# Kernel tuning notes

Hardware: AMD Instinct MI355X
Metric: run time of the kernel (lower is better)

The kernel has to match this reference:

```python
import jax, jax.numpy as jnp
import numpy as np

D_MODEL = 768
N_HEADS = 12
D_K = D_MODEL // N_HEADS
NEG_INF = -1e9


def setup_inputs() -> dict:
    key = jax.random.key(0)
    ks = jax.random.split(key, 7)
    B, S = 4, 2048
    x = jax.random.normal(ks[0], (B, S, D_MODEL), dtype=jnp.float32)
    # causal mask, broadcastable to [B, H, S, S]
    mask = jnp.tril(jnp.ones((S, S), dtype=bool))[None, None, :, :]
    scale = 1.0 / np.sqrt(D_MODEL)
    Wq = jax.random.normal(ks[1], (D_MODEL, D_MODEL), dtype=jnp.float32) * scale
    bq = jnp.zeros((D_MODEL,), dtype=jnp.float32)
    Wk = jax.random.normal(ks[2], (D_MODEL, D_MODEL), dtype=jnp.float32) * scale
    bk = jnp.zeros((D_MODEL,), dtype=jnp.float32)
    Wv = jax.random.normal(ks[3], (D_MODEL, D_MODEL), dtype=jnp.float32) * scale
    bv = jnp.zeros((D_MODEL,), dtype=jnp.float32)
    return {"x": x, "mask": mask, "Wq": Wq, "bq": bq, "Wk": Wk, "bk": bk, "Wv": Wv, "bv": bv}


def reference(x, mask, Wq, bq, Wk, bk, Wv, bv):
    B, S, _ = x.shape
    # projections (torch Linear: y = x @ W.T + b)
    q = (x @ Wq.T + bq).reshape(B, S, N_HEADS, D_K)
    k = (x @ Wk.T + bk).reshape(B, S, N_HEADS, D_K)
    v = (x @ Wv.T + bv).reshape(B, S, N_HEADS, D_K)
    # scores: [B, H, S, S]
    scores = jnp.einsum("bqhd,bkhd->bhqk", q, k) / jnp.sqrt(jnp.float32(D_K))
    scores = jnp.where(mask, scores, NEG_INF)
    probs = jax.nn.softmax(scores, axis=-1)
    # attention: [B, H, S, D_K] -> [B, S, d_model]
    attn = jnp.einsum("bhqk,bkhd->bqhd", probs, v).reshape(B, S, D_MODEL)
    return attn
```

## Files before the change

### kernel.cpp

```cpp
#include <hip/hip_runtime.h>


#define S_LEN 2048
#define BATCH 4
#define HEADS 12
#define DM 768
#define DK 64
#define BH (BATCH*HEADS)
#define MROWS (BATCH*S_LEN)

typedef __attribute__((ext_vector_type(8))) short short8;
typedef __attribute__((ext_vector_type(4))) float floatx4;
typedef __attribute__((address_space(3))) unsigned char lds_byte;
typedef __attribute__((address_space(1))) const unsigned char glob_byte;

__device__ __forceinline__ unsigned short f2bf(float f) {
  union { float f; unsigned int u; } a; a.f = f;
  unsigned int u = a.u;
  return (unsigned short)((u + 0x7fffu + ((u >> 16) & 1u)) >> 16);
}

__global__ void cast_f32_bf16(const float* __restrict__ src,
                              unsigned short* __restrict__ dst, int n) {
  int i = (blockIdx.x * blockDim.x + threadIdx.x) * 4;
  if (i < n) {
    float4 v = *(const float4*)(src + i);
    ushort4 o;
    o.x = f2bf(v.x); o.y = f2bf(v.y); o.z = f2bf(v.z); o.w = f2bf(v.w);
    *(ushort4*)(dst + i) = o;
  }
}

__global__ void cast_w3(const float* __restrict__ w0, const float* __restrict__ w1,
                        const float* __restrict__ w2, unsigned short* __restrict__ dst,
                        int n) {
  const float* src = (blockIdx.y == 0) ? w0 : (blockIdx.y == 1) ? w1 : w2;
  int i = (blockIdx.x * blockDim.x + threadIdx.x) * 4;
  if (i < n) {
    float4 v = *(const float4*)(src + i);
    ushort4 o;
    o.x = f2bf(v.x); o.y = f2bf(v.y); o.z = f2bf(v.z); o.w = f2bf(v.w);
    *(ushort4*)(dst + (size_t)blockIdx.y * n + i) = o;
  }
}

__global__ __launch_bounds__(256) void qkv_gemm(
    const unsigned short* __restrict__ xb,
    const unsigned short* __restrict__ wb,
    const float* __restrict__ bq, const float* __restrict__ bk,
    const float* __restrict__ bv,
    unsigned short* __restrict__ qo,
    unsigned short* __restrict__ ko,
    unsigned short* __restrict__ vto) {
  __shared__ unsigned short a_lds[128 * 32];
  __shared__ unsigned short b_lds[128 * 32];
  const int mat = blockIdx.z;
  const int tid = threadIdx.x;
  const int wave = tid >> 6, lane = tid & 63, quad = lane >> 4, ln = lane & 15;
  const int wm = wave & 1, wn = wave >> 1;
  const int m_blk = blockIdx.x * 128, n_blk = blockIdx.y * 128;
  const unsigned short* w = wb + (size_t)mat * DM * DM;

  const int srow = lane >> 2, schunk = lane & 3;

  const floatx4 fz = {0.f, 0.f, 0.f, 0.f};
  floatx4 acc[4][4];
#pragma unroll
  for (int mg = 0; mg < 4; mg++)
#pragma unroll
    for (int c = 0; c < 4; c++) acc[mg][c] = fz;

  for (int k0 = 0; k0 < DM; k0 += 32) {
#pragma unroll
    for (int j = 0; j < 2; j++) {
      int row = wave * 32 + j * 16 + srow;
      __builtin_amdgcn_global_load_lds(
          (glob_byte*)(xb + (size_t)(m_blk + row) * DM + k0 + schunk * 8),
          (lds_byte*)(a_lds + (size_t)(wave * 32 + j * 16) * 32), 16, 0, 0);
      __builtin_amdgcn_global_load_lds(
          (glob_byte*)(w + (size_t)(n_blk + row) * DM + k0 + schunk * 8),
          (lds_byte*)(b_lds + (size_t)(wave * 32 + j * 16) * 32), 16, 0, 0);
    }
    __syncthreads();

    short8 af[4], bf[4];
#pragma unroll
    for (int mg = 0; mg < 4; mg++)
      af[mg] = *(const short8*)(a_lds + (wm * 64 + mg * 16 + ln) * 32 + quad * 8);
#pragma unroll
    for (int c = 0; c < 4; c++)
      bf[c] = *(const short8*)(b_lds + (wn * 64 + c * 16 + ln) * 32 + quad * 8);
#pragma unroll
    for (int mg = 0; mg < 4; mg++)
#pragma unroll
      for (int c = 0; c < 4; c++)
        acc[mg][c] = __builtin_amdgcn_mfma_f32_16x16x32_bf16(af[mg], bf[c], acc[mg][c], 0, 0, 0);
    __syncthreads();
  }

  const float* bias = (mat == 0) ? bq : (mat == 1) ? bk : bv;
  const int m_base = m_blk + wm * 64, n_base = n_blk + wn * 64;
#pragma unroll
  for (int mg = 0; mg < 4; mg++)
#pragma unroll
    for (int c = 0; c < 4; c++) {
      int gn = n_base + c * 16 + ln;
      int hd = gn >> 6, d = gn & 63;
      float bias_v = bias[gn];
      int gm0 = m_base + mg * 16 + quad * 4;
      int bb = gm0 >> 11, s0 = gm0 & (S_LEN - 1);
      if (mat == 2) {
        ushort4 pk;
        pk.x = f2bf(acc[mg][c][0] + bias_v);
        pk.y = f2bf(acc[mg][c][1] + bias_v);
        pk.z = f2bf(acc[mg][c][2] + bias_v);
        pk.w = f2bf(acc[mg][c][3] + bias_v);
        *(ushort4*)(vto + (((size_t)(bb * HEADS + hd)) * DK + d) * S_LEN + s0) = pk;
      } else {
        unsigned short* dst = (mat == 0 ? qo : ko) +
            (((size_t)(bb * HEADS + hd)) * S_LEN + s0) * DK + d;
#pragma unroll
        for (int r = 0; r < 4; r++)
          dst[(size_t)r * DK] = f2bf(acc[mg][c][r] + bias_v);
      }
    }
}

__global__ __launch_bounds__(128) void flash_attn(
    const unsigned short* __restrict__ q,
    const unsigned short* __restrict__ k,
    const unsigned short* __restrict__ vt,
    float* __restrict__ out) {
  __shared__ unsigned short p_lds[2][32 * 64];
  const int id = blockIdx.x;
  const int bh = id % BH;
  const int qt = (S_LEN / 64 - 1) - (id / BH);
  const int q0 = qt * 64;
  const int tid = threadIdx.x;
  const int wave = tid >> 6, lane = tid & 63, quad = lane >> 4, ln = lane & 15;
  unsigned short* pl = p_lds[wave];
  const unsigned short* qp = q  + (size_t)bh * S_LEN * DK;
  const unsigned short* kp = k  + (size_t)bh * S_LEN * DK;
  const unsigned short* vp = vt + (size_t)bh * DK * S_LEN;
  const int qr_base = q0 + wave * 32;

  short8 aq[2][2];
#pragma unroll
  for (int h = 0; h < 2; h++)
#pragma unroll
    for (int s = 0; s < 2; s++)
      aq[h][s] = *(const short8*)(qp + (size_t)(qr_base + h * 16 + ln) * DK + s * 32 + quad * 8);

  const floatx4 fz = {0.f, 0.f, 0.f, 0.f};
  floatx4 o[2][4];
  float l_part[2][4];
#pragma unroll
  for (int h = 0; h < 2; h++)
#pragma unroll
    for (int r = 0; r < 4; r++) {
      o[h][0] = fz; o[h][1] = fz; o[h][2] = fz; o[h][3] = fz;
      l_part[h][r] = 0.f;
    }

  const int kend = qr_base + 32;
  for (int k0 = 0; k0 < kend; k0 += 64) {
    short8 kf[4][2];
#pragma unroll
    for (int kg = 0; kg < 4; kg++)
#pragma unroll
      for (int s = 0; s < 2; s++)
        kf[kg][s] = *(const short8*)(kp + (size_t)(k0 + kg * 16 + ln) * DK + s * 32 + quad * 8);

    floatx4 sc[2][4];
#pragma unroll
    for (int h = 0; h < 2; h++)
#pragma unroll
      for (int kg = 0; kg < 4; kg++) {
        floatx4 t = __builtin_amdgcn_mfma_f32_16x16x32_bf16(aq[h][0], kf[kg][0], fz, 0, 0, 0);
        sc[h][kg] = __builtin_amdgcn_mfma_f32_16x16x32_bf16(aq[h][1], kf[kg][1], t, 0, 0, 0);
      }

    const bool domask = (k0 + 63 > qr_base);
#pragma unroll
    for (int h = 0; h < 2; h++) {
#pragma unroll
      for (int kg = 0; kg < 4; kg++) {
        int key = k0 + kg * 16 + ln;
#pragma unroll
        for (int r = 0; r < 4; r++) {
          float p = __expf(sc[h][kg][r] * 0.125f);
          if (domask) {
            int qr = qr_base + h * 16 + quad * 4 + r;
            p = (key <= qr) ? p : 0.f;
          }
          l_part[h][r] += p;
          int row = h * 16 + quad * 4 + r;
          int col = kg * 16 + ln;
          pl[row * 64 + (((col >> 3) ^ (row & 7)) * 8) + (col & 7)] = f2bf(p);
        }
      }
    }

    short8 ap[2][2];
#pragma unroll
    for (int h = 0; h < 2; h++)
#pragma unroll
      for (int s = 0; s < 2; s++)
        ap[h][s] = *(const short8*)(pl + (h * 16 + ln) * 64 + (((s * 4 + quad) ^ (ln & 7)) * 8));

    short8 vf[4][2];
#pragma unroll
    for (int dg = 0; dg < 4; dg++)
#pragma unroll
      for (int s = 0; s < 2; s++)
        vf[dg][s] = *(const short8*)(vp + (size_t)(dg * 16 + ln) * S_LEN + k0 + s * 32 + quad * 8);
#pragma unroll
    for (int h = 0; h < 2; h++)
#pragma unroll
      for (int dg = 0; dg < 4; dg++) {
        o[h][dg] = __builtin_amdgcn_mfma_f32_16x16x32_bf16(ap[h][0], vf[dg][0], o[h][dg], 0, 0, 0);
        o[h][dg] = __builtin_amdgcn_mfma_f32_16x16x32_bf16(ap[h][1], vf[dg][1], o[h][dg], 0, 0, 0);
      }
  }

  const int b = bh / HEADS, hd = bh % HEADS;
#pragma unroll
  for (int h = 0; h < 2; h++)
#pragma unroll
    for (int r = 0; r < 4; r++) {
      float l = l_part[h][r];
      l += __shfl_xor(l, 1);
      l += __shfl_xor(l, 2);
      l += __shfl_xor(l, 4);
      l += __shfl_xor(l, 8);
      float inv = 1.f / l;
      int qr = qr_base + h * 16 + quad * 4 + r;
      float* orow = out + ((size_t)(b * S_LEN + qr)) * DM + hd * DK;
      orow[ln]      = o[h][0][r] * inv;
      orow[16 + ln] = o[h][1][r] * inv;
      orow[32 + ln] = o[h][2][r] * inv;
      orow[48 + ln] = o[h][3][r] * inv;
    }
}

extern "C" void kernel_launch(void* const* d_in, const int* in_sizes, int n_in,
                              void* d_out, int out_size, void* d_ws, size_t ws_size,
                              hipStream_t stream) {
  const float* x  = (const float*)d_in[0];
  const float* Wq = (const float*)d_in[2];
  const float* bq = (const float*)d_in[3];
  const float* Wk = (const float*)d_in[4];
  const float* bk = (const float*)d_in[5];
  const float* Wv = (const float*)d_in[6];
  const float* bv = (const float*)d_in[7];
  float* out = (float*)d_out;

  const int NX = MROWS * DM;
  const int NW = DM * DM;
  unsigned short* xb = (unsigned short*)d_ws;
  unsigned short* wb = xb + NX;
  unsigned short* qo = wb + 3 * NW;
  unsigned short* ko = qo + (size_t)BH * S_LEN * DK;
  unsigned short* vt = ko + (size_t)BH * S_LEN * DK;

  cast_f32_bf16<<<(NX / 4 + 255) / 256, 256, 0, stream>>>(x, xb, NX);
  cast_w3<<<dim3((NW / 4 + 255) / 256, 3), 256, 0, stream>>>(Wq, Wk, Wv, wb, NW);

  qkv_gemm<<<dim3(MROWS / 128, DM / 128, 3), 256, 0, stream>>>(
      xb, wb, bq, bk, bv, qo, ko, vt);

  flash_attn<<<dim3((S_LEN / 64) * BH), 128, 0, stream>>>(qo, ko, vt, out);
}
```

Baseline: 254.8 us.

## Fold softmax scale into Q, unroll attention loop with double-buffered P tiles

Pre-multiplies Q by log2(e)/sqrt(dk) in the projection epilogue so attention can use exp2f directly, removing a multiply per score. The attention key loop is refactored into an inlined step function, unrolled by two with separate per-wave P buffers in LDS, and the V loads are hoisted next to the K loads so both can be in flight together. Launch bounds now request 3 blocks per CU. The added register pressure from earlier V loads and the unroll may limit occupancy or cause spills. Q rounding to bf16 now happens after scaling, which changes numerics slightly.

```diff
diff --git a/kernel.cpp b/kernel.cpp
--- a/kernel.cpp
+++ b/kernel.cpp
@@ -1,4 +1,5 @@
 #include <hip/hip_runtime.h>
+#include <math.h>
 
 
 #define S_LEN 2048
@@ -8,6 +9,7 @@
 #define DK 64
 #define BH (BATCH*HEADS)
 #define MROWS (BATCH*S_LEN)
+#define QSCALE 0.1803368801111244f
 
 typedef __attribute__((ext_vector_type(8))) short short8;
 typedef __attribute__((ext_vector_type(4))) float floatx4;
@@ -60,7 +62,6 @@
   const int wm = wave & 1, wn = wave >> 1;
   const int m_blk = blockIdx.x * 128, n_blk = blockIdx.y * 128;
   const unsigned short* w = wb + (size_t)mat * DM * DM;
-
   const int srow = lane >> 2, schunk = lane & 3;
 
   const floatx4 fz = {0.f, 0.f, 0.f, 0.f};
@@ -99,6 +100,7 @@
   }
 
   const float* bias = (mat == 0) ? bq : (mat == 1) ? bk : bv;
+  const float oscale = (mat == 0) ? QSCALE : 1.0f;
   const int m_base = m_blk + wm * 64, n_base = n_blk + wn * 64;
 #pragma unroll
   for (int mg = 0; mg < 4; mg++)
@@ -106,7 +108,7 @@
     for (int c = 0; c < 4; c++) {
       int gn = n_base + c * 16 + ln;
       int hd = gn >> 6, d = gn & 63;
-      float bias_v = bias[gn];
+      float bias_v = bias[gn] * oscale;
       int gm0 = m_base + mg * 16 + quad * 4;
       int bb = gm0 >> 11, s0 = gm0 & (S_LEN - 1);
       if (mat == 2) {
@@ -121,24 +123,86 @@
             (((size_t)(bb * HEADS + hd)) * S_LEN + s0) * DK + d;
 #pragma unroll
         for (int r = 0; r < 4; r++)
-          dst[(size_t)r * DK] = f2bf(acc[mg][c][r] + bias_v);
+          dst[(size_t)r * DK] = f2bf(acc[mg][c][r] * oscale + bias_v);
       }
     }
 }
 
-__global__ __launch_bounds__(128) void flash_attn(
+__device__ __forceinline__ void attn_step(
+    int k0, int qr_base, int quad, int ln,
+    const unsigned short* __restrict__ kp, const unsigned short* __restrict__ vp,
+    unsigned short* __restrict__ pl,
+    const short8 (&aq)[2][2], floatx4 (&o)[2][4], float (&l_part)[2][4]) {
+  const floatx4 fz = {0.f, 0.f, 0.f, 0.f};
+  short8 kf[4][2], vf[4][2];
+#pragma unroll
+  for (int kg = 0; kg < 4; kg++)
+#pragma unroll
+    for (int s = 0; s < 2; s++) {
+      kf[kg][s] = *(const short8*)(kp + (size_t)(k0 + kg * 16 + ln) * DK + s * 32 + quad * 8);
+      vf[kg][s] = *(const short8*)(vp + (size_t)(kg * 16 + ln) * S_LEN + k0 + s * 32 + quad * 8);
+    }
+
+  floatx4 sc[2][4];
+#pragma unroll
+  for (int h = 0; h < 2; h++)
+#pragma unroll
+    for (int kg = 0; kg < 4; kg++) {
+      floatx4 t = __builtin_amdgcn_mfma_f32_16x16x32_bf16(aq[h][0], kf[kg][0], fz, 0, 0, 0);
+      sc[h][kg] = __builtin_amdgcn_mfma_f32_16x16x32_bf16(aq[h][1], kf[kg][1], t, 0, 0, 0);
+    }
+
+  const bool domask = (k0 + 63 > qr_base);
+#pragma unroll
+  for (int h = 0; h < 2; h++) {
+#pragma unroll
+    for (int kg = 0; kg < 4; kg++) {
+      int key = k0 + kg * 16 + ln;
+#pragma unroll
+      for (int r = 0; r < 4; r++) {
+        float p = exp2f(sc[h][kg][r]);
+        if (domask) {
+          int qr = qr_base + h * 16 + quad * 4 + r;
+          p = (key <= qr) ? p : 0.f;
+        }
+        l_part[h][r] += p;
+        int row = h * 16 + quad * 4 + r;
+        int col = kg * 16 + ln;
+        pl[row * 64 + (((col >> 3) ^ (row & 7)) * 8) + (col & 7)] = f2bf(p);
+      }
+    }
+  }
+
+  short8 ap[2][2];
+#pragma unroll
+  for (int h = 0; h < 2; h++)
+#pragma unroll
+    for (int s = 0; s < 2; s++)
+      ap[h][s] = *(const short8*)(pl + (h * 16 + ln) * 64 + (((s * 4 + quad) ^ (ln & 7)) * 8));
+
+#pragma unroll
+  for (int h = 0; h < 2; h++)
+#pragma unroll
+    for (int dg = 0; dg < 4; dg++) {
+      o[h][dg] = __builtin_amdgcn_mfma_f32_16x16x32_bf16(ap[h][0], vf[dg][0], o[h][dg], 0, 0, 0);
+      o[h][dg] = __builtin_amdgcn_mfma_f32_16x16x32_bf16(ap[h][1], vf[dg][1], o[h][dg], 0, 0, 0);
+    }
+}
+
+__global__ __launch_bounds__(128, 3) void flash_attn(
     const unsigned short* __restrict__ q,
     const unsigned short* __restrict__ k,
     const unsigned short* __restrict__ vt,
     float* __restrict__ out) {
-  __shared__ unsigned short p_lds[2][32 * 64];
+  __shared__ unsigned short p_lds[2][2][32 * 64];
   const int id = blockIdx.x;
   const int bh = id % BH;
   const int qt = (S_LEN / 64 - 1) - (id / BH);
   const int q0 = qt * 64;
   const int tid = threadIdx.x;
   const int wave = tid >> 6, lane = tid & 63, quad = lane >> 4, ln = lane & 15;
-  unsigned short* pl = p_lds[wave];
+  unsigned short* pl0 = p_lds[wave][0];
+  unsigned short* pl1 = p_lds[wave][1];
   const unsigned short* qp = q  + (size_t)bh * S_LEN * DK;
   const unsigned short* kp = k  + (size_t)bh * S_LEN * DK;
   const unsigned short* vp = vt + (size_t)bh * DK * S_LEN;
@@ -163,65 +227,14 @@
     }
 
   const int kend = qr_base + 32;
-  for (int k0 = 0; k0 < kend; k0 += 64) {
-    short8 kf[4][2];
-#pragma unroll
-    for (int kg = 0; kg < 4; kg++)
-#pragma unroll
-      for (int s = 0; s < 2; s++)
-        kf[kg][s] = *(const short8*)(kp + (size_t)(k0 + kg * 16 + ln) * DK + s * 32 + quad * 8);
-
-    floatx4 sc[2][4];
-#pragma unroll
-    for (int h = 0; h < 2; h++)
-#pragma unroll
-      for (int kg = 0; kg < 4; kg++) {
-        floatx4 t = __builtin_amdgcn_mfma_f32_16x16x32_bf16(aq[h][0], kf[kg][0], fz, 0, 0, 0);
-        sc[h][kg] = __builtin_amdgcn_mfma_f32_16x16x32_bf16(aq[h][1], kf[kg][1], t, 0, 0, 0);
-      }
-
-    const bool domask = (k0 + 63 > qr_base);
-#pragma unroll
-    for (int h = 0; h < 2; h++) {
-#pragma unroll
-      for (int kg = 0; kg < 4; kg++) {
-        int key = k0 + kg * 16 + ln;
-#pragma unroll
-        for (int r = 0; r < 4; r++) {
-          float p = __expf(sc[h][kg][r] * 0.125f);
-          if (domask) {
-            int qr = qr_base + h * 16 + quad * 4 + r;
-            p = (key <= qr) ? p : 0.f;
-          }
-          l_part[h][r] += p;
-          int row = h * 16 + quad * 4 + r;
-          int col = kg * 16 + ln;
-          pl[row * 64 + (((col >> 3) ^ (row & 7)) * 8) + (col & 7)] = f2bf(p);
-        }
-      }
-    }
-
-    short8 ap[2][2];
-#pragma unroll
-    for (int h = 0; h < 2; h++)
-#pragma unroll
-      for (int s = 0; s < 2; s++)
-        ap[h][s] = *(const short8*)(pl + (h * 16 + ln) * 64 + (((s * 4 + quad) ^ (ln & 7)) * 8));
-
-    short8 vf[4][2];
-#pragma unroll
-    for (int dg = 0; dg < 4; dg++)
-#pragma unroll
-      for (int s = 0; s < 2; s++)
-        vf[dg][s] = *(const short8*)(vp + (size_t)(dg * 16 + ln) * S_LEN + k0 + s * 32 + quad * 8);
-#pragma unroll
-    for (int h = 0; h < 2; h++)
-#pragma unroll
-      for (int dg = 0; dg < 4; dg++) {
-        o[h][dg] = __builtin_amdgcn_mfma_f32_16x16x32_bf16(ap[h][0], vf[dg][0], o[h][dg], 0, 0, 0);
-        o[h][dg] = __builtin_amdgcn_mfma_f32_16x16x32_bf16(ap[h][1], vf[dg][1], o[h][dg], 0, 0, 0);
-      }
-  }
+  int k0 = 0;
+  while (k0 + 128 <= kend) {
+    attn_step(k0,      qr_base, quad, ln, kp, vp, pl0, aq, o, l_part);
+    attn_step(k0 + 64, qr_base, quad, ln, kp, vp, pl1, aq, o, l_part);
+    k0 += 128;
+  }
+  for (int t = 0; k0 < kend; k0 += 64, t ^= 1)
+    attn_step(k0, qr_base, quad, ln, kp, vp, t ? pl1 : pl0, aq, o, l_part);
 
   const int b = bh / HEADS, hd = bh % HEADS;
 #pragma unroll
```

New measurement: 392.5 us. +54.0%, slower.

## Schedule attention tiles per wave via atomic queue and fold softmax scale into Q

Applied to the files above, without the earlier changes.

The attention kernel now hands out 32-row causal query tiles to individual waves. Each wave takes its next tile from a global atomic counter, longest tiles first, instead of each block owning a fixed 64-row tile, which is meant to even out the causal work imbalance and the tail. The 1/sqrt(dk)*log2(e) factor is folded into the Q projection epilogue, so the softmax uses exp2f with no per-element multiply. This adds one memset launch and one atomic per tile. The larger scale on Q may slightly change bf16 rounding of Q.

```diff
diff --git a/kernel.cpp b/kernel.cpp
--- a/kernel.cpp
+++ b/kernel.cpp
@@ -1,4 +1,5 @@
 #include <hip/hip_runtime.h>
+#include <math.h>
 
 
 #define S_LEN 2048
@@ -8,6 +9,8 @@
 #define DK 64
 #define BH (BATCH*HEADS)
 #define MROWS (BATCH*S_LEN)
+#define QSCALE 0.1803368801111244f
+#define N_ITEMS ((S_LEN/32)*BH)
 
 typedef __attribute__((ext_vector_type(8))) short short8;
 typedef __attribute__((ext_vector_type(4))) float floatx4;
@@ -60,7 +63,6 @@
   const int wm = wave & 1, wn = wave >> 1;
   const int m_blk = blockIdx.x * 128, n_blk = blockIdx.y * 128;
   const unsigned short* w = wb + (size_t)mat * DM * DM;
-
   const int srow = lane >> 2, schunk = lane & 3;
 
   const floatx4 fz = {0.f, 0.f, 0.f, 0.f};
@@ -99,6 +101,7 @@
   }
 
   const float* bias = (mat == 0) ? bq : (mat == 1) ? bk : bv;
+  const float oscale = (mat == 0) ? QSCALE : 1.0f;
   const int m_base = m_blk + wm * 64, n_base = n_blk + wn * 64;
 #pragma unroll
   for (int mg = 0; mg < 4; mg++)
@@ -106,7 +109,7 @@
     for (int c = 0; c < 4; c++) {
       int gn = n_base + c * 16 + ln;
       int hd = gn >> 6, d = gn & 63;
-      float bias_v = bias[gn];
+      float bias_v = bias[gn] * oscale;
       int gm0 = m_base + mg * 16 + quad * 4;
       int bb = gm0 >> 11, s0 = gm0 & (S_LEN - 1);
       if (mat == 2) {
@@ -121,7 +124,7 @@
             (((size_t)(bb * HEADS + hd)) * S_LEN + s0) * DK + d;
 #pragma unroll
         for (int r = 0; r < 4; r++)
-          dst[(size_t)r * DK] = f2bf(acc[mg][c][r] + bias_v);
+          dst[(size_t)r * DK] = f2bf(acc[mg][c][r] * oscale + bias_v);
       }
     }
 }
@@ -130,117 +133,124 @@
     const unsigned short* __restrict__ q,
     const unsigned short* __restrict__ k,
     const unsigned short* __restrict__ vt,
-    float* __restrict__ out) {
+    float* __restrict__ out,
+    unsigned int* __restrict__ work_ctr) {
   __shared__ unsigned short p_lds[2][32 * 64];
-  const int id = blockIdx.x;
-  const int bh = id % BH;
-  const int qt = (S_LEN / 64 - 1) - (id / BH);
-  const int q0 = qt * 64;
   const int tid = threadIdx.x;
   const int wave = tid >> 6, lane = tid & 63, quad = lane >> 4, ln = lane & 15;
   unsigned short* pl = p_lds[wave];
-  const unsigned short* qp = q  + (size_t)bh * S_LEN * DK;
-  const unsigned short* kp = k  + (size_t)bh * S_LEN * DK;
-  const unsigned short* vp = vt + (size_t)bh * DK * S_LEN;
-  const int qr_base = q0 + wave * 32;
-
-  short8 aq[2][2];
-#pragma unroll
-  for (int h = 0; h < 2; h++)
-#pragma unroll
-    for (int s = 0; s < 2; s++)
-      aq[h][s] = *(const short8*)(qp + (size_t)(qr_base + h * 16 + ln) * DK + s * 32 + quad * 8);
-
   const floatx4 fz = {0.f, 0.f, 0.f, 0.f};
-  floatx4 o[2][4];
-  float l_part[2][4];
-#pragma unroll
-  for (int h = 0; h < 2; h++)
-#pragma unroll
-    for (int r = 0; r < 4; r++) {
-      o[h][0] = fz; o[h][1] = fz; o[h][2] = fz; o[h][3] = fz;
-      l_part[h][r] = 0.f;
+
+  for (;;) {
+    unsigned int item = 0;
+    if (lane == 0) item = atomicAdd(work_ctr, 1u);
+    item = __shfl((int)item, 0);
+    if (item >= N_ITEMS) return;
+
+    const int bh = item % BH;
+    const int t  = (S_LEN / 32 - 1) - (int)(item / BH);
+    const int qr_base = t * 32;
+    const unsigned short* qp = q  + (size_t)bh * S_LEN * DK;
+    const unsigned short* kp = k  + (size_t)bh * S_LEN * DK;
+    const unsigned short* vp = vt + (size_t)bh * DK * S_LEN;
+
+    short8 aq[2][2];
+#pragma unroll
+    for (int h = 0; h < 2; h++)
+#pragma unroll
+      for (int s = 0; s < 2; s++)
+        aq[h][s] = *(const short8*)(qp + (size_t)(qr_base + h * 16 + ln) * DK + s * 32 + quad * 8);
+
+    floatx4 o[2][4];
+    float l_part[2][4];
+#pragma unroll
+    for (int h = 0; h < 2; h++)
+#pragma unroll
+      for (int r = 0; r < 4; r++) {
+        o[h][0] = fz; o[h][1] = fz; o[h][2] = fz; o[h][3] = fz;
+        l_part[h][r] = 0.f;
+      }
+
+    const int kend = qr_base + 32;
+    for (int k0 = 0; k0 < kend; k0 += 64) {
+      short8 kf[4][2];
+#pragma unroll
+      for (int kg = 0; kg < 4; kg++)
+#pragma unroll
+        for (int s = 0; s < 2; s++)
+          kf[kg][s] = *(const short8*)(kp + (size_t)(k0 + kg * 16 + ln) * DK + s * 32 + quad * 8);
+
+      floatx4 sc[2][4];
+#pragma unroll
+      for (int h = 0; h < 2; h++)
+#pragma unroll
+        for (int kg = 0; kg < 4; kg++) {
+          floatx4 tt = __builtin_amdgcn_mfma_f32_16x16x32_bf16(aq[h][0], kf[kg][0], fz, 0, 0, 0);
+          sc[h][kg] = __builtin_amdgcn_mfma_f32_16x16x32_bf16(aq[h][1], kf[kg][1], tt, 0, 0, 0);
+        }
+
+      const bool domask = (k0 + 63 > qr_base);
+#pragma unroll
+      for (int h = 0; h < 2; h++) {
+#pragma unroll
+        for (int kg = 0; kg < 4; kg++) {
+          int key = k0 + kg * 16 + ln;
+#pragma unroll
+          for (int r = 0; r < 4; r++) {
+            float p = exp2f(sc[h][kg][r]);
+            if (domask) {
+              int qr = qr_base + h * 16 + quad * 4 + r;
+              p = (key <= qr) ? p : 0.f;
+            }
+            l_part[h][r] += p;
+            int row = h * 16 + quad * 4 + r;
+            int col = kg * 16 + ln;
+            pl[row * 64 + (((col >> 3) ^ (row & 7)) * 8) + (col & 7)] = f2bf(p);
+          }
+        }
+      }
+
+      short8 ap[2][2];
+#pragma unroll
+      for (int h = 0; h < 2; h++)
+#pragma unroll
+        for (int s = 0; s < 2; s++)
+          ap[h][s] = *(const short8*)(pl + (h * 16 + ln) * 64 + (((s * 4 + quad) ^ (ln & 7)) * 8));
+
+      short8 vf[4][2];
+#pragma unroll
+      for (int dg = 0; dg < 4; dg++)
+#pragma unroll
+        for (int s = 0; s < 2; s++)
+          vf[dg][s] = *(const short8*)(vp + (size_t)(dg * 16 + ln) * S_LEN + k0 + s * 32 + quad * 8);
+#pragma unroll
+      for (int h = 0; h < 2; h++)
+#pragma unroll
+        for (int dg = 0; dg < 4; dg++) {
+          o[h][dg] = __builtin_amdgcn_mfma_f32_16x16x32_bf16(ap[h][0], vf[dg][0], o[h][dg], 0, 0, 0);
+          o[h][dg] = __builtin_amdgcn_mfma_f32_16x16x32_bf16(ap[h][1], vf[dg][1], o[h][dg], 0, 0, 0);
+        }
     }
 
-  const int kend = qr_base + 32;
-  for (int k0 = 0; k0 < kend; k0 += 64) {
-    short8 kf[4][2];
-#pragma unroll
-    for (int kg = 0; kg < 4; kg++)
-#pragma unroll
-      for (int s = 0; s < 2; s++)
-        kf[kg][s] = *(const short8*)(kp + (size_t)(k0 + kg * 16 + ln) * DK + s * 32 + quad * 8);
-
-    floatx4 sc[2][4];
+    const int b = bh / HEADS, hd = bh % HEADS;
 #pragma unroll
     for (int h = 0; h < 2; h++)
 #pragma unroll
-      for (int kg = 0; kg < 4; kg++) {
-        floatx4 t = __builtin_amdgcn_mfma_f32_16x16x32_bf16(aq[h][0], kf[kg][0], fz, 0, 0, 0);
-        sc[h][kg] = __builtin_amdgcn_mfma_f32_16x16x32_bf16(aq[h][1], kf[kg][1], t, 0, 0, 0);
-      }
-
-    const bool domask = (k0 + 63 > qr_base);
-#pragma unroll
-    for (int h = 0; h < 2; h++) {
-#pragma unroll
-      for (int kg = 0; kg < 4; kg++) {
-        int key = k0 + kg * 16 + ln;
-#pragma unroll
-        for (int r = 0; r < 4; r++) {
-          float p = __expf(sc[h][kg][r] * 0.125f);
-          if (domask) {
-            int qr = qr_base + h * 16 + quad * 4 + r;
-            p = (key <= qr) ? p : 0.f;
-          }
-          l_part[h][r] += p;
-          int row = h * 16 + quad * 4 + r;
-          int col = kg * 16 + ln;
-          pl[row * 64 + (((col >> 3) ^ (row & 7)) * 8) + (col & 7)] = f2bf(p);
-        }
-      }
-    }
-
-    short8 ap[2][2];
-#pragma unroll
-    for (int h = 0; h < 2; h++)
-#pragma unroll
-      for (int s = 0; s < 2; s++)
-        ap[h][s] = *(const short8*)(pl + (h * 16 + ln) * 64 + (((s * 4 + quad) ^ (ln & 7)) * 8));
-
-    short8 vf[4][2];
-#pragma unroll
-    for (int dg = 0; dg < 4; dg++)
-#pragma unroll
-      for (int s = 0; s < 2; s++)
-        vf[dg][s] = *(const short8*)(vp + (size_t)(dg * 16 + ln) * S_LEN + k0 + s * 32 + quad * 8);
-#pragma unroll
-    for (int h = 0; h < 2; h++)
-#pragma unroll
-      for (int dg = 0; dg < 4; dg++) {
-        o[h][dg] = __builtin_amdgcn_mfma_f32_16x16x32_bf16(ap[h][0], vf[dg][0], o[h][dg], 0, 0, 0);
-        o[h][dg] = __builtin_amdgcn_mfma_f32_16x16x32_bf16(ap[h][1], vf[dg][1], o[h][dg], 0, 0, 0);
-      }
-  }
-
-  const int b = bh / HEADS, hd = bh % HEADS;
-#pragma unroll
-  for (int h = 0; h < 2; h++)
-#pragma unroll
-    for (int r = 0; r < 4; r++) {
-      float l = l_part[h][r];
-      l += __shfl_xor(l, 1);
-      l += __shfl_xor(l, 2);
-      l += __shfl_xor(l, 4);
-      l += __shfl_xor(l, 8);
-      float inv = 1.f / l;
-      int qr = qr_base + h * 16 + quad * 4 + r;
-      float* orow = out + ((size_t)(b * S_LEN + qr)) * DM + hd * DK;
-      orow[ln]      = o[h][0][r] * inv;
-      orow[16 + ln] = o[h][1][r] * inv;
-      orow[32 + ln] = o[h][2][r] * inv;
-      orow[48 + ln] = o[h][3][r] * inv;
-    }
+      for (int r = 0; r < 4; r++) {
+        float l = l_part[h][r];
+        l += __shfl_xor(l, 1);
+        l += __shfl_xor(l, 2);
+        l += __shfl_xor(l, 4);
+        l += __shfl_xor(l, 8);
+        float inv = 1.f / l;
+        int qr = qr_base + h * 16 + quad * 4 + r;
+        float* orow = out + ((size_t)(b * S_LEN + qr)) * DM + hd * DK;
+        orow[ln]      = o[h][0][r] * inv;
+        orow[16 + ln] = o[h][1][r] * inv;
+        orow[32 + ln] = o[h][2][r] * inv;
+        orow[48 + ln] = o[h][3][r] * inv;
+      }
+  }
 }
 
 extern "C" void kernel_launch(void* const* d_in, const int* in_sizes, int n_in,
@@ -262,6 +272,9 @@
   unsigned short* qo = wb + 3 * NW;
   unsigned short* ko = qo + (size_t)BH * S_LEN * DK;
   unsigned short* vt = ko + (size_t)BH * S_LEN * DK;
+  unsigned int* ctr = (unsigned int*)(vt + (size_t)BH * S_LEN * DK);
+
+  hipMemsetAsync(ctr, 0, sizeof(unsigned int), stream);
 
   cast_f32_bf16<<<(NX / 4 + 255) / 256, 256, 0, stream>>>(x, xb, NX);
   cast_w3<<<dim3((NW / 4 + 255) / 256, 3), 256, 0, stream>>>(Wq, Wk, Wv, wb, NW);
@@ -269,5 +282,5 @@
   qkv_gemm<<<dim3(MROWS / 128, DM / 128, 3), 256, 0, stream>>>(
       xb, wb, bq, bk, bv, qo, ko, vt);
 
-  flash_attn<<<dim3((S_LEN / 64) * BH), 128, 0, stream>>>(qo, ko, vt, out);
-}
+  flash_attn<<<dim3(N_ITEMS / 2), 128, 0, stream>>>(qo, ko, vt, out, ctr);
+}
```

New measurement: 305.8 us. 20.0% more time.

## Rebalance causal attention with paired 16-row tiles per wave and fold scale into Q

Applied to the files above, without the earlier changes.

Each wave now processes two 16-row query tiles, one short and one long (ti and 127-ti), so every wave does the same causal work. Heads are mapped across 768 blocks of 4 waves, grouped so that block-adjacent work shares a head. The softmax scale and log2(e) are folded into the Q projection so the inner loop uses exp2f directly. Probabilities are converted to bf16 by truncation rather than rounding. Using 16-row tiles halves K/V reuse per wave compared with 32-row tiles, which raises global load traffic.

```diff
diff --git a/kernel.cpp b/kernel.cpp
--- a/kernel.cpp
+++ b/kernel.cpp
@@ -1,4 +1,5 @@
 #include <hip/hip_runtime.h>
+#include <math.h>
 
 
 #define S_LEN 2048
@@ -8,6 +9,7 @@
 #define DK 64
 #define BH (BATCH*HEADS)
 #define MROWS (BATCH*S_LEN)
+#define QSCALE 0.1803368801111244f
 
 typedef __attribute__((ext_vector_type(8))) short short8;
 typedef __attribute__((ext_vector_type(4))) float floatx4;
@@ -18,6 +20,10 @@
   union { float f; unsigned int u; } a; a.f = f;
   unsigned int u = a.u;
   return (unsigned short)((u + 0x7fffu + ((u >> 16) & 1u)) >> 16);
+}
+__device__ __forceinline__ unsigned short f2bf_rtz(float f) {
+  union { float f; unsigned int u; } a; a.f = f;
+  return (unsigned short)(a.u >> 16);
 }
 
 __global__ void cast_f32_bf16(const float* __restrict__ src,
@@ -60,7 +66,6 @@
   const int wm = wave & 1, wn = wave >> 1;
   const int m_blk = blockIdx.x * 128, n_blk = blockIdx.y * 128;
   const unsigned short* w = wb + (size_t)mat * DM * DM;
-
   const int srow = lane >> 2, schunk = lane & 3;
 
   const floatx4 fz = {0.f, 0.f, 0.f, 0.f};
@@ -99,6 +104,7 @@
   }
 
   const float* bias = (mat == 0) ? bq : (mat == 1) ? bk : bv;
+  const float oscale = (mat == 0) ? QSCALE : 1.0f;
   const int m_base = m_blk + wm * 64, n_base = n_blk + wn * 64;
 #pragma unroll
   for (int mg = 0; mg < 4; mg++)
@@ -106,7 +112,7 @@
     for (int c = 0; c < 4; c++) {
       int gn = n_base + c * 16 + ln;
       int hd = gn >> 6, d = gn & 63;
-      float bias_v = bias[gn];
+      float bias_v = bias[gn] * oscale;
       int gm0 = m_base + mg * 16 + quad * 4;
       int bb = gm0 >> 11, s0 = gm0 & (S_LEN - 1);
       if (mat == 2) {
@@ -121,126 +127,112 @@
             (((size_t)(bb * HEADS + hd)) * S_LEN + s0) * DK + d;
 #pragma unroll
         for (int r = 0; r < 4; r++)
-          dst[(size_t)r * DK] = f2bf(acc[mg][c][r] + bias_v);
-      }
-    }
-}
-
-__global__ __launch_bounds__(128) void flash_attn(
+          dst[(size_t)r * DK] = f2bf(acc[mg][c][r] * oscale + bias_v);
+      }
+    }
+}
+
+__global__ __launch_bounds__(256) void flash_attn(
     const unsigned short* __restrict__ q,
     const unsigned short* __restrict__ k,
     const unsigned short* __restrict__ vt,
     float* __restrict__ out) {
-  __shared__ unsigned short p_lds[2][32 * 64];
-  const int id = blockIdx.x;
-  const int bh = id % BH;
-  const int qt = (S_LEN / 64 - 1) - (id / BH);
-  const int q0 = qt * 64;
+  __shared__ unsigned short p_lds[4][16 * 64];
   const int tid = threadIdx.x;
   const int wave = tid >> 6, lane = tid & 63, quad = lane >> 4, ln = lane & 15;
   unsigned short* pl = p_lds[wave];
+  const int g = blockIdx.x & 7;
+  const int s = blockIdx.x >> 3;
+  const int p = s * 4 + wave;
+  const int bh = g + 8 * (p % 6);
+  const int ti = p / 6;
   const unsigned short* qp = q  + (size_t)bh * S_LEN * DK;
   const unsigned short* kp = k  + (size_t)bh * S_LEN * DK;
   const unsigned short* vp = vt + (size_t)bh * DK * S_LEN;
-  const int qr_base = q0 + wave * 32;
-
-  short8 aq[2][2];
-#pragma unroll
-  for (int h = 0; h < 2; h++)
-#pragma unroll
-    for (int s = 0; s < 2; s++)
-      aq[h][s] = *(const short8*)(qp + (size_t)(qr_base + h * 16 + ln) * DK + s * 32 + quad * 8);
-
   const floatx4 fz = {0.f, 0.f, 0.f, 0.f};
-  floatx4 o[2][4];
-  float l_part[2][4];
-#pragma unroll
-  for (int h = 0; h < 2; h++)
-#pragma unroll
-    for (int r = 0; r < 4; r++) {
-      o[h][0] = fz; o[h][1] = fz; o[h][2] = fz; o[h][3] = fz;
-      l_part[h][r] = 0.f;
-    }
-
-  const int kend = qr_base + 32;
-  for (int k0 = 0; k0 < kend; k0 += 64) {
-    short8 kf[4][2];
-#pragma unroll
-    for (int kg = 0; kg < 4; kg++)
-#pragma unroll
-      for (int s = 0; s < 2; s++)
-        kf[kg][s] = *(const short8*)(kp + (size_t)(k0 + kg * 16 + ln) * DK + s * 32 + quad * 8);
-
-    floatx4 sc[2][4];
-#pragma unroll
-    for (int h = 0; h < 2; h++)
+  const int b = bh / HEADS, hd = bh % HEADS;
+
+#pragma unroll
+  for (int job = 0; job < 2; job++) {
+    const int t16 = job ? (127 - ti) : ti;
+    const int qr_base = t16 * 16;
+
+    short8 aq[2];
+#pragma unroll
+    for (int ss = 0; ss < 2; ss++)
+      aq[ss] = *(const short8*)(qp + (size_t)(qr_base + ln) * DK + ss * 32 + quad * 8);
+
+    floatx4 o[4] = {fz, fz, fz, fz};
+    float l_part[4] = {0.f, 0.f, 0.f, 0.f};
+
+    const int kend = qr_base + 16;
+    for (int k0 = 0; k0 < kend; k0 += 64) {
+      short8 kf[4][2];
+#pragma unroll
+      for (int kg = 0; kg < 4; kg++)
+#pragma unroll
+        for (int ss = 0; ss < 2; ss++)
+          kf[kg][ss] = *(const short8*)(kp + (size_t)(k0 + kg * 16 + ln) * DK + ss * 32 + quad * 8);
+
+      floatx4 sc[4];
 #pragma unroll
       for (int kg = 0; kg < 4; kg++) {
-        floatx4 t = __builtin_amdgcn_mfma_f32_16x16x32_bf16(aq[h][0], kf[kg][0], fz, 0, 0, 0);
-        sc[h][kg] = __builtin_amdgcn_mfma_f32_16x16x32_bf16(aq[h][1], kf[kg][1], t, 0, 0, 0);
-      }
-
-    const bool domask = (k0 + 63 > qr_base);
-#pragma unroll
-    for (int h = 0; h < 2; h++) {
+        floatx4 tt = __builtin_amdgcn_mfma_f32_16x16x32_bf16(aq[0], kf[kg][0], fz, 0, 0, 0);
+        sc[kg] = __builtin_amdgcn_mfma_f32_16x16x32_bf16(aq[1], kf[kg][1], tt, 0, 0, 0);
+      }
+
+      const bool domask = (k0 + 63 > qr_base);
 #pragma unroll
       for (int kg = 0; kg < 4; kg++) {
         int key = k0 + kg * 16 + ln;
 #pragma unroll
         for (int r = 0; r < 4; r++) {
-          float p = __expf(sc[h][kg][r] * 0.125f);
+          float pv = exp2f(sc[kg][r]);
           if (domask) {
-            int qr = qr_base + h * 16 + quad * 4 + r;
-            p = (key <= qr) ? p : 0.f;
+            int qr = qr_base + quad * 4 + r;
+            pv = (key <= qr) ? pv : 0.f;
           }
-          l_part[h][r] += p;
-          int row = h * 16 + quad * 4 + r;
+          l_part[r] += pv;
+          int row = quad * 4 + r;
           int col = kg * 16 + ln;
-          pl[row * 64 + (((col >> 3) ^ (row & 7)) * 8) + (col & 7)] = f2bf(p);
+          pl[row * 64 + (((col >> 3) ^ row) & 7) * 8 + (col & 7)] = f2bf_rtz(pv);
         }
       }
-    }
-
-    short8 ap[2][2];
-#pragma unroll
-    for (int h = 0; h < 2; h++)
-#pragma unroll
-      for (int s = 0; s < 2; s++)
-        ap[h][s] = *(const short8*)(pl + (h * 16 + ln) * 64 + (((s * 4 + quad) ^ (ln & 7)) * 8));
-
-    short8 vf[4][2];
-#pragma unroll
-    for (int dg = 0; dg < 4; dg++)
-#pragma unroll
-      for (int s = 0; s < 2; s++)
-        vf[dg][s] = *(const short8*)(vp + (size_t)(dg * 16 + ln) * S_LEN + k0 + s * 32 + quad * 8);
-#pragma unroll
-    for (int h = 0; h < 2; h++)
+
+      short8 ap[2];
+#pragma unroll
+      for (int ss = 0; ss < 2; ss++)
+        ap[ss] = *(const short8*)(pl + ln * 64 + (((ss * 4 + quad) ^ ln) & 7) * 8);
+
+      short8 vf[4][2];
+#pragma unroll
+      for (int dg = 0; dg < 4; dg++)
+#pragma unroll
+        for (int ss = 0; ss < 2; ss++)
+          vf[dg][ss] = *(const short8*)(vp + (size_t)(dg * 16 + ln) * S_LEN + k0 + ss * 32 + quad * 8);
 #pragma unroll
       for (int dg = 0; dg < 4; dg++) {
-        o[h][dg] = __builtin_amdgcn_mfma_f32_16x16x32_bf16(ap[h][0], vf[dg][0], o[h][dg], 0, 0, 0);
-        o[h][dg] = __builtin_amdgcn_mfma_f32_16x16x32_bf16(ap[h][1], vf[dg][1], o[h][dg], 0, 0, 0);
-      }
-  }
-
-  const int b = bh / HEADS, hd = bh % HEADS;
-#pragma unroll
-  for (int h = 0; h < 2; h++)
+        o[dg] = __builtin_amdgcn_mfma_f32_16x16x32_bf16(ap[0], vf[dg][0], o[dg], 0, 0, 0);
+        o[dg] = __builtin_amdgcn_mfma_f32_16x16x32_bf16(ap[1], vf[dg][1], o[dg], 0, 0, 0);
+      }
+    }
+
 #pragma unroll
     for (int r = 0; r < 4; r++) {
-      float l = l_part[h][r];
+      float l = l_part[r];
       l += __shfl_xor(l, 1);
       l += __shfl_xor(l, 2);
       l += __shfl_xor(l, 4);
       l += __shfl_xor(l, 8);
       float inv = 1.f / l;
-      int qr = qr_base + h * 16 + quad * 4 + r;
+      int qr = qr_base + quad * 4 + r;
       float* orow = out + ((size_t)(b * S_LEN + qr)) * DM + hd * DK;
-      orow[ln]      = o[h][0][r] * inv;
-      orow[16 + ln] = o[h][1][r] * inv;
-      orow[32 + ln] = o[h][2][r] * inv;
-      orow[48 + ln] = o[h][3][r] * inv;
-    }
+      orow[ln]      = o[0][r] * inv;
+      orow[16 + ln] = o[1][r] * inv;
+      orow[32 + ln] = o[2][r] * inv;
+      orow[48 + ln] = o[3][r] * inv;
+    }
+  }
 }
 
 extern "C" void kernel_launch(void* const* d_in, const int* in_sizes, int n_in,
@@ -269,5 +261,5 @@
   qkv_gemm<<<dim3(MROWS / 128, DM / 128, 3), 256, 0, stream>>>(
       xb, wb, bq, bk, bv, qo, ko, vt);
 
-  flash_attn<<<dim3((S_LEN / 64) * BH), 128, 0, stream>>>(qo, ko, vt, out);
-}
+  flash_attn<<<dim3(768), 256, 0, stream>>>(qo, ko, vt, out);
+}
```

Measured after the change: 331.6 us. 1.3x slower.
